# Optimization experiments

Hardware: AMD Instinct MI355X
Metric: run time of the kernel (lower is better)

The kernel has to match this reference:

```python
import jax, jax.numpy as jnp
import numpy as np

S, B, D, H, HD = 2048, 1, 1280, 16, 80
NSEQ = 8  # packed sequences

def setup_inputs() -> dict:
    key = jax.random.key(0)
    k1, k2, k3 = jax.random.split(key, 3)
    x = jax.random.normal(k1, (S, B, D), dtype=jnp.float32)
    # cu_seqlens: 8 equal packed segments, starts at 0, ends at S
    cu_seqlens = (jnp.arange(NSEQ + 1, dtype=jnp.int32) * (S // NSEQ))
    W_qkv = jax.random.normal(k2, (3 * D, D), dtype=jnp.float32) * (1.0 / np.sqrt(D))
    b_qkv = jax.random.normal(k3, (3 * D,), dtype=jnp.float32) * 0.01
    return {"x": x, "cu_seqlens": cu_seqlens, "W_qkv": W_qkv, "b_qkv": b_qkv}

def _block_diag_mask(cu_seqlens, s):
    # segment id of each position; positions in the same segment attend to each other
    pos = jnp.arange(s)
    seg = jnp.searchsorted(cu_seqlens[1:], pos, side='right')  # [s]
    return seg[:, None] == seg[None, :]  # [s, s] bool

def reference(x, cu_seqlens, W_qkv, b_qkv):
    s, b, d = x.shape
    qkv = jnp.einsum('sbd,ed->sbe', x, W_qkv) + b_qkv  # [s,b,3d]
    q, k, v = jnp.split(qkv, 3, axis=2)
    # [s,b,h,hd] -> [b,h,s,hd]
    def to_bhsd(t):
        return t.reshape(s, b, H, HD).transpose(1, 2, 0, 3)
    q1, k1, v1 = to_bhsd(q), to_bhsd(k), to_bhsd(v)
    mask = _block_diag_mask(cu_seqlens, s)  # [s,s]
    scale = 1.0 / np.sqrt(HD)
    scores = jnp.einsum('bhsd,bhtd->bhst', q1, k1) * scale  # [b,h,s,s]
    neg = jnp.finfo(scores.dtype).min
    scores = jnp.where(mask[None, None, :, :], scores, neg)
    attn = jax.nn.softmax(scores, axis=-1)
    out = jnp.einsum('bhst,bhtd->bhsd', attn, v1)  # [b,h,s,hd]
    return out.transpose(0, 2, 1, 3)  # [b,s,h,hd]
```

## Files before the change

kernel.cpp:

```cpp
#include <hip/hip_runtime.h>
#include <hip/hip_bf16.h>

#define S_LEN 2048
#define DIM 1280
#define NH 16
#define HD 80
#define NE 3840
#define SEG 256
#define NSEG 8
#define QKV_SZ (NH * S_LEN * HD)
#define NX (S_LEN * DIM)
#define NW (NE * DIM)

typedef short short8 __attribute__((ext_vector_type(8)));
typedef float floatx4 __attribute__((ext_vector_type(4)));

__device__ inline unsigned short f2bf(float f) {
    unsigned int u = __float_as_uint(f);
    return (unsigned short)((u + 0x7fffu + ((u >> 16) & 1u)) >> 16);
}

__global__ __launch_bounds__(256) void convert_bf16_kernel(
    const float* __restrict__ x, const float* __restrict__ W,
    unsigned short* __restrict__ xb, unsigned short* __restrict__ Wb)
{
    const int gi = blockIdx.x * 256 + threadIdx.x;
    const float* src;
    unsigned short* dst;
    int off;
    if (gi < NX / 4) { src = x; dst = xb; off = gi * 4; }
    else             { src = W; dst = Wb; off = (gi - NX / 4) * 4; }
    float4 v = *(const float4*)(src + off);
    ushort4 o;
    o.x = f2bf(v.x); o.y = f2bf(v.y); o.z = f2bf(v.z); o.w = f2bf(v.w);
    *(ushort4*)(dst + off) = o;
}

#define GLLS(gp, lp) __builtin_amdgcn_global_load_lds( \
    (const __attribute__((address_space(1))) unsigned int*)(gp), \
    (__attribute__((address_space(3))) unsigned int*)(lp), 16, 0, 0)
#define BAR  __builtin_amdgcn_s_barrier()
#define FEN  asm volatile("" ::: "memory")
#define SB0  __builtin_amdgcn_sched_barrier(0)
#define LGKM0 asm volatile("s_waitcnt lgkmcnt(0)" ::: "memory")

#define PHASE(cb, nb, ktn, kk, WAITS, PF) do { \
    asm volatile("s_waitcnt vmcnt(" WAITS ")" ::: "memory"); \
    BAR; FEN; \
    _Pragma("unroll") \
    for (int mi = 0; mi < 4; ++mi) \
        aF[mi] = *(const short8*)&(cb)[(kk) * 4096 + (wr * 64 + mi * 16 + lm) * 32 + swzb]; \
    _Pragma("unroll") \
    for (int ni = 0; ni < 4; ++ni) \
        bF[ni] = *(const short8*)&(cb)[8192 + (kk) * 4096 + (wc * 64 + ni * 16 + lm) * 32 + swzb]; \
    if (PF) { \
        GLLS(agA0 + (ktn) * 64 + (kk) * 32, (nb) + (kk) * 4096 + tid * 8); \
        GLLS(agA1 + (ktn) * 64 + (kk) * 32, (nb) + (kk) * 4096 + 2048 + tid * 8); \
        GLLS(bgp0 + (ktn) * 64 + (kk) * 32, (nb) + 8192 + (kk) * 4096 + tid * 8); \
        GLLS(bgp1 + (ktn) * 64 + (kk) * 32, (nb) + 8192 + (kk) * 4096 + 2048 + tid * 8); \
    } \
    BAR; FEN; LGKM0; SB0; \
    __builtin_amdgcn_s_setprio(1); \
    _Pragma("unroll") \
    for (int mi = 0; mi < 4; ++mi) \
        _Pragma("unroll") \
        for (int ni = 0; ni < 4; ++ni) \
            acc[mi][ni] = __builtin_amdgcn_mfma_f32_16x16x32_bf16( \
                aF[mi], bF[ni], acc[mi][ni], 0, 0, 0); \
    __builtin_amdgcn_s_setprio(0); \
} while (0)

__global__ __launch_bounds__(256) void qkv_gemm_kernel(
    const unsigned short* __restrict__ xb,
    const unsigned short* __restrict__ Wb,
    const float* __restrict__ bias,
    unsigned short* __restrict__ qkvb)
{
    __shared__ short smem[32768];

    const int tid  = threadIdx.x;
    const int wid  = tid >> 6;
    const int lane = tid & 63;
    const int quad = lane >> 4;
    const int lm   = lane & 15;
    const int wr   = wid >> 1;
    const int wc   = wid & 1;

    const int bid = blockIdx.x;
    const int xcd = bid & 7;
    const int j   = bid >> 3;
    const int bm  = (xcd & 3) * 4 + (j & 3);
    const int bn  = (xcd >> 2) * 15 + (j >> 2);
    const int m0  = bm * 128;
    const int n0  = bn * 128;

    const int srow = tid >> 2;
    const int kblk = ((tid & 3) ^ ((tid >> 3) & 3)) * 8;
    const unsigned short* agA0 = xb + (size_t)(m0 + srow) * DIM + kblk;
    const unsigned short* agA1 = xb + (size_t)(m0 + 64 + srow) * DIM + kblk;
    const unsigned short* bgp0 = Wb + (size_t)(n0 + srow) * DIM + kblk;
    const unsigned short* bgp1 = Wb + (size_t)(n0 + 64 + srow) * DIM + kblk;

    const int swzb = (quad ^ ((lm >> 1) & 3)) * 8;

    floatx4 acc[4][4];
    #pragma unroll
    for (int mi = 0; mi < 4; ++mi)
        #pragma unroll
        for (int ni = 0; ni < 4; ++ni)
            acc[mi][ni] = (floatx4){0.f, 0.f, 0.f, 0.f};

    GLLS(agA0,      smem + tid * 8);
    GLLS(agA1,      smem + 2048 + tid * 8);
    GLLS(bgp0,      smem + 8192 + tid * 8);
    GLLS(bgp1,      smem + 8192 + 2048 + tid * 8);
    GLLS(agA0 + 32, smem + 4096 + tid * 8);
    GLLS(agA1 + 32, smem + 4096 + 2048 + tid * 8);
    GLLS(bgp0 + 32, smem + 12288 + tid * 8);
    GLLS(bgp1 + 32, smem + 12288 + 2048 + tid * 8);

    short8 aF[4], bF[4];

    for (int kt = 0; kt < 19; ++kt) {
        const short* cb = smem + (kt & 1) * 16384;
        short* nb = smem + ((kt & 1) ^ 1) * 16384;
        PHASE(cb, nb, kt + 1, 0, "4", 1);
        PHASE(cb, nb, kt + 1, 1, "4", 1);
    }
    {
        const short* cb = smem + 16384;
        short* nb = smem;
        PHASE(cb, nb, 0, 0, "4", 0);
        PHASE(cb, nb, 0, 1, "0", 0);
    }

    const int which = n0 / DIM;
    const int nrembase = n0 - which * DIM + wc * 64;
    const int rowb = m0 + wr * 64;

    #pragma unroll
    for (int ni = 0; ni < 4; ++ni) {
        const int nrem = nrembase + ni * 16 + lm;
        const float bv = bias[which * DIM + nrem];
        const int hh = nrem / HD;
        const int hd = nrem - hh * HD;
        if (which < 2) {
            unsigned short* hp = qkvb + (size_t)which * QKV_SZ
                               + (size_t)hh * (S_LEN * HD) + hd;
            #pragma unroll
            for (int mi = 0; mi < 4; ++mi) {
                const int mb = rowb + mi * 16 + quad * 4;
                #pragma unroll
                for (int r = 0; r < 4; ++r)
                    hp[(size_t)(mb + r) * HD] = f2bf(acc[mi][ni][r] + bv);
            }
        } else {
            unsigned short* hp = qkvb + 2 * (size_t)QKV_SZ
                               + (size_t)hh * (HD * S_LEN) + (size_t)hd * S_LEN;
            #pragma unroll
            for (int mi = 0; mi < 4; ++mi) {
                const int mb = rowb + mi * 16 + quad * 4;
                #pragma unroll
                for (int r = 0; r < 4; ++r)
                    hp[mb + r] = f2bf(acc[mi][ni][r] + bv);
            }
        }
    }
}

__global__ __launch_bounds__(256) void attn_kernel(
    const unsigned short* __restrict__ Qb,
    const unsigned short* __restrict__ Kb,
    const unsigned short* __restrict__ Vb,
    float* __restrict__ out)
{
    __shared__ short KVs[128 * 104];
    __shared__ short Ps[64 * 136];
    __shared__ float rsl[4][64];

    const int qc  = blockIdx.x;
    const int h   = blockIdx.y;
    const int seg = blockIdx.z;
    const int tid = threadIdx.x;
    const int w    = tid >> 6;
    const int lane = tid & 63;
    const int quad = lane >> 4;
    const int lm   = lane & 15;
    const int qbase = seg * SEG + qc * 64;
    const float scale2 = 0.16130930362690808f;
    const short8 zfrag = {0, 0, 0, 0, 0, 0, 0, 0};

    int kkey[5], kc[5], vhd[5], vsc[5];
    #pragma unroll
    for (int rnd = 0; rnd < 5; ++rnd) {
        const int f = rnd * 256 + tid;
        kkey[rnd] = f / 10;
        kc[rnd]   = f - kkey[rnd] * 10;
        vhd[rnd]  = f >> 4;
        vsc[rnd]  = f & 15;
    }

    short8 aQ[4][3];
    #pragma unroll
    for (int mt = 0; mt < 4; ++mt) {
        const unsigned short* qp = Qb + ((size_t)h * S_LEN + qbase + mt * 16 + lm) * HD;
        #pragma unroll
        for (int ks = 0; ks < 3; ++ks) {
            const int hd0 = ks * 32 + quad * 8;
            aQ[mt][ks] = (hd0 < 80) ? *(const short8*)(qp + hd0) : zfrag;
        }
    }

    short8 Kreg[5], Vreg[5];
    {
        const unsigned short* src = Kb + ((size_t)h * S_LEN + seg * SEG) * HD;
        #pragma unroll
        for (int rnd = 0; rnd < 5; ++rnd)
            Kreg[rnd] = *(const short8*)(src + kkey[rnd] * 80 + kc[rnd] * 8);
    }

    floatx4 Oacc[5];
    #pragma unroll
    for (int nt = 0; nt < 5; ++nt) Oacc[nt] = (floatx4){0.f, 0.f, 0.f, 0.f};
    float rsp[4][4];
    #pragma unroll
    for (int mt = 0; mt < 4; ++mt)
        #pragma unroll
        for (int r = 0; r < 4; ++r) rsp[mt][r] = 0.0f;

    for (int half = 0; half < 2; ++half) {
        const int k0g = seg * SEG + half * 128;

        __syncthreads();

        #pragma unroll
        for (int rnd = 0; rnd < 5; ++rnd)
            *(short8*)&KVs[kkey[rnd] * 104 + kc[rnd] * 8] = Kreg[rnd];
        {
            const int zkey = tid >> 1;
            const int zc = tid & 1;
            *(short8*)&KVs[zkey * 104 + 80 + zc * 8] = zfrag;
        }

        {
            const unsigned short* src = Vb + (size_t)h * (HD * S_LEN) + k0g;
            #pragma unroll
            for (int rnd = 0; rnd < 5; ++rnd)
                Vreg[rnd] = *(const short8*)(src + vhd[rnd] * S_LEN + vsc[rnd] * 8);
        }
        __syncthreads();

        floatx4 Cs[4][2];
        #pragma unroll
        for (int mt = 0; mt < 4; ++mt)
            #pragma unroll
            for (int nt = 0; nt < 2; ++nt) Cs[mt][nt] = (floatx4){0.f, 0.f, 0.f, 0.f};

        #pragma unroll
        for (int ks = 0; ks < 3; ++ks) {
            short8 b[2];
            #pragma unroll
            for (int nt = 0; nt < 2; ++nt)
                b[nt] = *(const short8*)&KVs[(w * 32 + nt * 16 + lm) * 104 + ks * 32 + quad * 8];
            #pragma unroll
            for (int mt = 0; mt < 4; ++mt)
                #pragma unroll
                for (int nt = 0; nt < 2; ++nt)
                    Cs[mt][nt] = __builtin_amdgcn_mfma_f32_16x16x32_bf16(
                        aQ[mt][ks], b[nt], Cs[mt][nt], 0, 0, 0);
        }

        #pragma unroll
        for (int mt = 0; mt < 4; ++mt)
            #pragma unroll
            for (int nt = 0; nt < 2; ++nt)
                #pragma unroll
                for (int r = 0; r < 4; ++r) {
                    const float p = __builtin_amdgcn_exp2f(Cs[mt][nt][r] * scale2);
                    rsp[mt][r] += p;
                    Ps[(mt * 16 + quad * 4 + r) * 136 + w * 32 + nt * 16 + lm]
                        = (short)f2bf(p);
                }
        __syncthreads();

        #pragma unroll
        for (int rnd = 0; rnd < 5; ++rnd)
            *(short8*)&KVs[vhd[rnd] * 136 + vsc[rnd] * 8] = Vreg[rnd];

        if (half == 0) {
            const unsigned short* src = Kb + ((size_t)h * S_LEN + seg * SEG + 128) * HD;
            #pragma unroll
            for (int rnd = 0; rnd < 5; ++rnd)
                Kreg[rnd] = *(const short8*)(src + kkey[rnd] * 80 + kc[rnd] * 8);
        }
        __syncthreads();

        #pragma unroll
        for (int ks2 = 0; ks2 < 4; ++ks2) {
            const short8 a = *(const short8*)&Ps[(w * 16 + lm) * 136 + ks2 * 32 + quad * 8];
            #pragma unroll
            for (int nt = 0; nt < 5; ++nt) {
                const short8 b = *(const short8*)&KVs[(nt * 16 + lm) * 136 + ks2 * 32 + quad * 8];
                Oacc[nt] = __builtin_amdgcn_mfma_f32_16x16x32_bf16(a, b, Oacc[nt], 0, 0, 0);
            }
        }
    }

    #pragma unroll
    for (int mt = 0; mt < 4; ++mt)
        #pragma unroll
        for (int r = 0; r < 4; ++r) {
            float v = rsp[mt][r];
            v += __shfl_xor(v, 1);
            v += __shfl_xor(v, 2);
            v += __shfl_xor(v, 4);
            v += __shfl_xor(v, 8);
            if (lm == 0) rsl[w][mt * 16 + quad * 4 + r] = v;
        }
    __syncthreads();

    #pragma unroll
    for (int r = 0; r < 4; ++r) {
        const int row = w * 16 + quad * 4 + r;
        const float l = rsl[0][row] + rsl[1][row] + rsl[2][row] + rsl[3][row];
        const float linv = 1.0f / l;
        float* op = out + (size_t)(qbase + row) * (NH * HD) + h * HD;
        #pragma unroll
        for (int nt = 0; nt < 5; ++nt)
            op[nt * 16 + lm] = Oacc[nt][r] * linv;
    }
}

extern "C" void kernel_launch(void* const* d_in, const int* in_sizes, int n_in,
                              void* d_out, int out_size, void* d_ws, size_t ws_size,
                              hipStream_t stream)
{
    const float* x      = (const float*)d_in[0];
    const float* W_qkv  = (const float*)d_in[2];
    const float* b_qkv  = (const float*)d_in[3];
    float* out = (float*)d_out;

    unsigned short* xb = (unsigned short*)d_ws;
    unsigned short* Wb = xb + NX;
    unsigned short* qkvb = Wb + NW;
    unsigned short* Qb = qkvb;
    unsigned short* Kb = qkvb + QKV_SZ;
    unsigned short* Vb = qkvb + 2 * (size_t)QKV_SZ;

    convert_bf16_kernel<<<(NX + NW) / 4 / 256, 256, 0, stream>>>(x, W_qkv, xb, Wb);
    qkv_gemm_kernel<<<480, 256, 0, stream>>>(xb, Wb, b_qkv, qkvb);
    attn_kernel<<<dim3(4, NH, NSEG), 256, 0, stream>>>(Qb, Kb, Vb, out);
}
```

Measured before the change: 124.1 us.

## Enlarge QKV GEMM tile to 256x128 with triple-buffered 32-wide K stages

The QKV GEMM block tile grows from 128x128 to 256x128, so each wave computes 128x64 and B fragments are reused across twice as many MFMAs. The LDS pipeline changes from a double buffer of 64-wide K tiles to a three-stage ring of 32-wide K tiles with a two-stage prefetch distance. The grid shrinks to 240 blocks, with launch bounds asking for two blocks per CU. This aims to cut LDS and global load traffic per FLOP, at the cost of more accumulator registers and fewer blocks than CUs, which may leave part of the GPU idle.

New measurement: 121.9 us. About the same (-1.7%).

```diff
diff --git a/kernel.cpp b/kernel.cpp
--- a/kernel.cpp
+++ b/kernel.cpp
@@ -44,25 +44,27 @@
 #define SB0  __builtin_amdgcn_sched_barrier(0)
 #define LGKM0 asm volatile("s_waitcnt lgkmcnt(0)" ::: "memory")
 
-#define PHASE(cb, nb, ktn, kk, WAITS, PF) do { \
+#define KTILE(cbo, nbo, ktn, WAITS, PF) do { \
     asm volatile("s_waitcnt vmcnt(" WAITS ")" ::: "memory"); \
     BAR; FEN; \
     _Pragma("unroll") \
-    for (int mi = 0; mi < 4; ++mi) \
-        aF[mi] = *(const short8*)&(cb)[(kk) * 4096 + (wr * 64 + mi * 16 + lm) * 32 + swzb]; \
+    for (int mi = 0; mi < 8; ++mi) \
+        aF[mi] = *(const short8*)&smem[(cbo) + (wr * 128 + mi * 16 + lm) * 32 + swzb]; \
     _Pragma("unroll") \
     for (int ni = 0; ni < 4; ++ni) \
-        bF[ni] = *(const short8*)&(cb)[8192 + (kk) * 4096 + (wc * 64 + ni * 16 + lm) * 32 + swzb]; \
+        bF[ni] = *(const short8*)&smem[(cbo) + 8192 + (wc * 64 + ni * 16 + lm) * 32 + swzb]; \
     if (PF) { \
-        GLLS(agA0 + (ktn) * 64 + (kk) * 32, (nb) + (kk) * 4096 + tid * 8); \
-        GLLS(agA1 + (ktn) * 64 + (kk) * 32, (nb) + (kk) * 4096 + 2048 + tid * 8); \
-        GLLS(bgp0 + (ktn) * 64 + (kk) * 32, (nb) + 8192 + (kk) * 4096 + tid * 8); \
-        GLLS(bgp1 + (ktn) * 64 + (kk) * 32, (nb) + 8192 + (kk) * 4096 + 2048 + tid * 8); \
+        GLLS(agA0 + (ktn) * 32, smem + (nbo) + tid * 8); \
+        GLLS(agA1 + (ktn) * 32, smem + (nbo) + 2048 + tid * 8); \
+        GLLS(agA2 + (ktn) * 32, smem + (nbo) + 4096 + tid * 8); \
+        GLLS(agA3 + (ktn) * 32, smem + (nbo) + 6144 + tid * 8); \
+        GLLS(bgp0 + (ktn) * 32, smem + (nbo) + 8192 + tid * 8); \
+        GLLS(bgp1 + (ktn) * 32, smem + (nbo) + 8192 + 2048 + tid * 8); \
     } \
     BAR; FEN; LGKM0; SB0; \
     __builtin_amdgcn_s_setprio(1); \
     _Pragma("unroll") \
-    for (int mi = 0; mi < 4; ++mi) \
+    for (int mi = 0; mi < 8; ++mi) \
         _Pragma("unroll") \
         for (int ni = 0; ni < 4; ++ni) \
             acc[mi][ni] = __builtin_amdgcn_mfma_f32_16x16x32_bf16( \
@@ -70,13 +72,13 @@
     __builtin_amdgcn_s_setprio(0); \
 } while (0)
 
-__global__ __launch_bounds__(256) void qkv_gemm_kernel(
+__global__ __launch_bounds__(256, 2) void qkv_gemm_kernel(
     const unsigned short* __restrict__ xb,
     const unsigned short* __restrict__ Wb,
     const float* __restrict__ bias,
     unsigned short* __restrict__ qkvb)
 {
-    __shared__ short smem[32768];
+    __shared__ short smem[36864];
 
     const int tid  = threadIdx.x;
     const int wid  = tid >> 6;
@@ -89,54 +91,57 @@
     const int bid = blockIdx.x;
     const int xcd = bid & 7;
     const int j   = bid >> 3;
-    const int bm  = (xcd & 3) * 4 + (j & 3);
-    const int bn  = (xcd >> 2) * 15 + (j >> 2);
-    const int m0  = bm * 128;
+    const int bm  = (xcd & 3) * 2 + (j & 1);
+    const int bn  = (xcd >> 2) * 15 + (j >> 1);
+    const int m0  = bm * 256;
     const int n0  = bn * 128;
 
     const int srow = tid >> 2;
     const int kblk = ((tid & 3) ^ ((tid >> 3) & 3)) * 8;
     const unsigned short* agA0 = xb + (size_t)(m0 + srow) * DIM + kblk;
     const unsigned short* agA1 = xb + (size_t)(m0 + 64 + srow) * DIM + kblk;
+    const unsigned short* agA2 = xb + (size_t)(m0 + 128 + srow) * DIM + kblk;
+    const unsigned short* agA3 = xb + (size_t)(m0 + 192 + srow) * DIM + kblk;
     const unsigned short* bgp0 = Wb + (size_t)(n0 + srow) * DIM + kblk;
     const unsigned short* bgp1 = Wb + (size_t)(n0 + 64 + srow) * DIM + kblk;
 
     const int swzb = (quad ^ ((lm >> 1) & 3)) * 8;
 
-    floatx4 acc[4][4];
-    #pragma unroll
-    for (int mi = 0; mi < 4; ++mi)
+    floatx4 acc[8][4];
+    #pragma unroll
+    for (int mi = 0; mi < 8; ++mi)
         #pragma unroll
         for (int ni = 0; ni < 4; ++ni)
             acc[mi][ni] = (floatx4){0.f, 0.f, 0.f, 0.f};
 
     GLLS(agA0,      smem + tid * 8);
     GLLS(agA1,      smem + 2048 + tid * 8);
+    GLLS(agA2,      smem + 4096 + tid * 8);
+    GLLS(agA3,      smem + 6144 + tid * 8);
     GLLS(bgp0,      smem + 8192 + tid * 8);
     GLLS(bgp1,      smem + 8192 + 2048 + tid * 8);
-    GLLS(agA0 + 32, smem + 4096 + tid * 8);
-    GLLS(agA1 + 32, smem + 4096 + 2048 + tid * 8);
-    GLLS(bgp0 + 32, smem + 12288 + tid * 8);
-    GLLS(bgp1 + 32, smem + 12288 + 2048 + tid * 8);
-
-    short8 aF[4], bF[4];
-
-    for (int kt = 0; kt < 19; ++kt) {
-        const short* cb = smem + (kt & 1) * 16384;
-        short* nb = smem + ((kt & 1) ^ 1) * 16384;
-        PHASE(cb, nb, kt + 1, 0, "4", 1);
-        PHASE(cb, nb, kt + 1, 1, "4", 1);
-    }
-    {
-        const short* cb = smem + 16384;
-        short* nb = smem;
-        PHASE(cb, nb, 0, 0, "4", 0);
-        PHASE(cb, nb, 0, 1, "0", 0);
-    }
+    GLLS(agA0 + 32, smem + 12288 + tid * 8);
+    GLLS(agA1 + 32, smem + 12288 + 2048 + tid * 8);
+    GLLS(agA2 + 32, smem + 12288 + 4096 + tid * 8);
+    GLLS(agA3 + 32, smem + 12288 + 6144 + tid * 8);
+    GLLS(bgp0 + 32, smem + 12288 + 8192 + tid * 8);
+    GLLS(bgp1 + 32, smem + 12288 + 8192 + 2048 + tid * 8);
+
+    short8 aF[8], bF[4];
+
+    int cbo = 0, nbo = 24576;
+    for (int kt = 0; kt < 38; ++kt) {
+        KTILE(cbo, nbo, kt + 2, "6", 1);
+        cbo = (cbo == 24576) ? 0 : cbo + 12288;
+        nbo = (nbo == 24576) ? 0 : nbo + 12288;
+    }
+    KTILE(cbo, nbo, 0, "6", 0);
+    cbo = (cbo == 24576) ? 0 : cbo + 12288;
+    KTILE(cbo, nbo, 0, "0", 0);
 
     const int which = n0 / DIM;
     const int nrembase = n0 - which * DIM + wc * 64;
-    const int rowb = m0 + wr * 64;
+    const int rowb = m0 + wr * 128;
 
     #pragma unroll
     for (int ni = 0; ni < 4; ++ni) {
@@ -148,7 +153,7 @@
             unsigned short* hp = qkvb + (size_t)which * QKV_SZ
                                + (size_t)hh * (S_LEN * HD) + hd;
             #pragma unroll
-            for (int mi = 0; mi < 4; ++mi) {
+            for (int mi = 0; mi < 8; ++mi) {
                 const int mb = rowb + mi * 16 + quad * 4;
                 #pragma unroll
                 for (int r = 0; r < 4; ++r)
@@ -158,7 +163,7 @@
             unsigned short* hp = qkvb + 2 * (size_t)QKV_SZ
                                + (size_t)hh * (HD * S_LEN) + (size_t)hd * S_LEN;
             #pragma unroll
-            for (int mi = 0; mi < 4; ++mi) {
+            for (int mi = 0; mi < 8; ++mi) {
                 const int mb = rowb + mi * 16 + quad * 4;
                 #pragma unroll
                 for (int r = 0; r < 4; ++r)
@@ -348,6 +353,6 @@
     unsigned short* Vb = qkvb + 2 * (size_t)QKV_SZ;
 
     convert_bf16_kernel<<<(NX + NW) / 4 / 256, 256, 0, stream>>>(x, W_qkv, xb, Wb);
-    qkv_gemm_kernel<<<480, 256, 0, stream>>>(xb, Wb, b_qkv, qkvb);
+    qkv_gemm_kernel<<<240, 256, 0, stream>>>(xb, Wb, b_qkv, qkvb);
     attn_kernel<<<dim3(4, NH, NSEG), 256, 0, stream>>>(Qb, Kb, Vb, out);
 }
```
